# Performance work log

Hardware: AMD Instinct MI355X
Metric: run time of the kernel (lower is better)

Reference implementation:

```python
import jax, jax.numpy as jnp
import numpy as np

ALPHA = 0.25
GAMMA = 2.0
EPS = 1e-8
W_CLASS = 2.0
W_BBOX = 5.0
W_GIOU = 2.0
B, Q, T, C = 64, 900, 300, 80


def setup_inputs() -> dict:
    key = jax.random.key(0)
    k1, k2, k3, k4 = jax.random.split(key, 4)
    pred_logits = jax.random.normal(k1, (B, Q, C), dtype=jnp.float32)
    pred_boxes = jax.random.uniform(k2, (B, Q, 4), dtype=jnp.float32)  # cxcywh in (0,1)
    tgt_labels = jax.random.randint(k3, (B, T), 0, C, dtype=jnp.int64)
    tgt_boxes = jax.random.uniform(k4, (B, T, 4), dtype=jnp.float32)
    return {"pred_logits": pred_logits, "pred_boxes": pred_boxes,
            "tgt_labels": tgt_labels, "tgt_boxes": tgt_boxes}


def box_cxcywh_to_xyxy(b):
    cx, cy, w, h = b[..., 0], b[..., 1], b[..., 2], b[..., 3]
    return jnp.stack([cx - 0.5 * w, cy - 0.5 * h, cx + 0.5 * w, cy + 0.5 * h], axis=-1)


def pairwise_giou(boxes1, boxes2):
    # boxes1: [B,Q,4] xyxy, boxes2: [B,T,4] xyxy -> [B,Q,T]
    area1 = (boxes1[..., 2] - boxes1[..., 0]) * (boxes1[..., 3] - boxes1[..., 1])
    area2 = (boxes2[..., 2] - boxes2[..., 0]) * (boxes2[..., 3] - boxes2[..., 1])
    lt = jnp.maximum(boxes1[:, :, None, :2], boxes2[:, None, :, :2])
    rb = jnp.minimum(boxes1[:, :, None, 2:], boxes2[:, None, :, 2:])
    wh = jnp.clip(rb - lt, 0.0)
    inter = wh[..., 0] * wh[..., 1]
    union = area1[:, :, None] + area2[:, None, :] - inter
    iou = inter / union
    lt_c = jnp.minimum(boxes1[:, :, None, :2], boxes2[:, None, :, :2])
    rb_c = jnp.maximum(boxes1[:, :, None, 2:], boxes2[:, None, :, 2:])
    wh_c = jnp.clip(rb_c - lt_c, 0.0)
    area_c = wh_c[..., 0] * wh_c[..., 1]
    return iou - (area_c - union) / area_c


def reference(pred_logits, pred_boxes, tgt_labels, tgt_boxes):
    # Batched cost matrix of HungarianMatcher (use_focal_loss=True).
    prob = jax.nn.sigmoid(pred_logits)  # [B,Q,C]
    idx = jnp.broadcast_to(tgt_labels[:, None, :], (prob.shape[0], prob.shape[1], tgt_labels.shape[1]))
    p = jnp.take_along_axis(prob, idx.astype(jnp.int32), axis=2)  # [B,Q,T]
    neg_cost = (1.0 - ALPHA) * p ** GAMMA * (-jnp.log(1.0 - p + EPS))
    pos_cost = ALPHA * (1.0 - p) ** GAMMA * (-jnp.log(p + EPS))
    cost_class = pos_cost - neg_cost
    cost_bbox = jnp.abs(pred_boxes[:, :, None, :] - tgt_boxes[:, None, :, :]).sum(-1)
    cost_giou = -pairwise_giou(box_cxcywh_to_xyxy(pred_boxes), box_cxcywh_to_xyxy(tgt_boxes))
    cost = W_BBOX * cost_bbox + W_CLASS * cost_class + W_GIOU * cost_giou
    return jnp.nan_to_num(cost, nan=1.0, posinf=1e6, neginf=-1e6)
```

## Files before the change

kernel.cpp:

```cpp
#include <hip/hip_runtime.h>


constexpr int B = 64, Q = 900, T = 300, C = 80;
constexpr int QTILE = 18;
constexpr int BLOCK = 256;
constexpr int TG    = T / 4;
constexpr int NIT   = (QTILE / 2) * TG;
constexpr float ALPHA = 0.25f;
constexpr float EPSF  = 1e-8f;

__device__ __forceinline__ float fast_rcp(float x) {
    return __builtin_amdgcn_rcpf(x);
}

__global__ __launch_bounds__(BLOCK) void matcher_cost_kernel(
    const float* __restrict__ logits,
    const float* __restrict__ pboxes,
    const int*   __restrict__ tlabels,
    const float* __restrict__ tboxes,
    float* __restrict__ out)
{
    __shared__ float4 s_t[9][TG];
    __shared__ int4   s_tl[TG];
    __shared__ float  s_cls[QTILE * C];
    __shared__ float4 s_pA[QTILE];
    __shared__ float4 s_pB[QTILE];

    const int bid = blockIdx.x;
    const int b   = bid / (Q / QTILE);
    const int q0  = (bid % (Q / QTILE)) * QTILE;
    const int tid = threadIdx.x;

    for (int t = tid; t < T; t += BLOCK) {
        float4 bx = *(const float4*)(tboxes + ((size_t)b * T + t) * 4);
        float x0 = bx.x - 0.5f * bx.z, y0 = bx.y - 0.5f * bx.w;
        float x1 = bx.x + 0.5f * bx.z, y1 = bx.y + 0.5f * bx.w;
        ((float*)&s_t[0][0])[t] = bx.x;
        ((float*)&s_t[1][0])[t] = bx.y;
        ((float*)&s_t[2][0])[t] = bx.z;
        ((float*)&s_t[3][0])[t] = bx.w;
        ((float*)&s_t[4][0])[t] = x0;
        ((float*)&s_t[5][0])[t] = y0;
        ((float*)&s_t[6][0])[t] = x1;
        ((float*)&s_t[7][0])[t] = y1;
        ((float*)&s_t[8][0])[t] = bx.z * bx.w;
        ((int*)&s_tl[0])[t]     = tlabels[(size_t)b * T + t];
    }

    if (tid < QTILE) {
        float4 bx = *(const float4*)(pboxes + ((size_t)b * Q + q0 + tid) * 4);
        float x0 = bx.x - 0.5f * bx.z, y0 = bx.y - 0.5f * bx.w;
        float x1 = bx.x + 0.5f * bx.z, y1 = bx.y + 0.5f * bx.w;
        s_pA[tid] = bx;
        s_pB[tid] = make_float4(x0, y0, x1, y1);
    }

    {
        const float* lg = logits + ((size_t)b * Q + q0) * C;
        for (int i = tid; i < QTILE * C; i += BLOCK) {
            float x  = lg[i];
            float pr = fast_rcp(1.0f + __expf(-x));
            float om = 1.0f - pr;
            float pos = ALPHA * om * om * (-__logf(pr + EPSF));
            float neg = (1.0f - ALPHA) * pr * pr * (-__logf(om + EPSF));
            s_cls[i] = 2.0f * (pos - neg) + 2.0f;
        }
    }

    __syncthreads();

    float* outb = out + ((size_t)b * Q + q0) * T;
    for (unsigned it = tid; it < NIT; it += BLOCK) {
        unsigned qp = it / TG;
        unsigned tg = it - qp * TG;

        float4 tcx = s_t[0][tg], tcy = s_t[1][tg];
        float4 tw  = s_t[2][tg], th  = s_t[3][tg];
        float4 tx0 = s_t[4][tg], ty0 = s_t[5][tg];
        float4 tx1 = s_t[6][tg], ty1 = s_t[7][tg];
        float4 ta  = s_t[8][tg];
        int4   lab = s_tl[tg];

        #pragma unroll
        for (int dq = 0; dq < 2; ++dq) {
            const int ql = qp * 2 + dq;
            float4 pA = s_pA[ql];
            float4 pB = s_pB[ql];
            float  pa = pA.z * pA.w;
            const float* clsrow = s_cls + ql * C;

            float4 res;
            #pragma unroll
            for (int k = 0; k < 4; ++k) {
                float tcx_ = (&tcx.x)[k], tcy_ = (&tcy.x)[k];
                float tw_  = (&tw.x)[k],  th_  = (&th.x)[k];
                float tx0_ = (&tx0.x)[k], ty0_ = (&ty0.x)[k];
                float tx1_ = (&tx1.x)[k], ty1_ = (&ty1.x)[k];
                float ta_  = (&ta.x)[k];

                float cbbox = (fabsf(pA.x - tcx_) + fabsf(pA.y - tcy_)) +
                              (fabsf(pA.z - tw_ ) + fabsf(pA.w - th_ ));
                float cls2 = clsrow[(&lab.x)[k]];

                float iw = fmaxf(fminf(pB.z, tx1_) - fmaxf(pB.x, tx0_), 0.0f);
                float ih = fmaxf(fminf(pB.w, ty1_) - fmaxf(pB.y, ty0_), 0.0f);
                float inter = iw * ih;
                float uni   = (pa + ta_) - inter;

                float cw = fmaxf(pB.z, tx1_) - fminf(pB.x, tx0_);
                float ch = fmaxf(pB.w, ty1_) - fminf(pB.y, ty0_);
                float ca = cw * ch;

                float num = fmaf(uni, uni, inter * ca);
                float r   = fast_rcp(uni * ca);
                float c   = fmaf(5.0f, cbbox, cls2);
                c = fmaf(num, -2.0f * r, c);

                if (c != c) c = 1.0f;

                (&res.x)[k] = c;
            }
            *(float4*)(outb + (size_t)ql * T + tg * 4) = res;
        }
    }
}

extern "C" void kernel_launch(void* const* d_in, const int* in_sizes, int n_in,
                              void* d_out, int out_size, void* d_ws, size_t ws_size,
                              hipStream_t stream) {
    const float* logits  = (const float*)d_in[0];
    const float* pboxes  = (const float*)d_in[1];
    const int*   tlabels = (const int*)  d_in[2];
    const float* tboxes  = (const float*)d_in[3];
    float* out = (float*)d_out;

    dim3 grid(B * (Q / QTILE));
    dim3 block(BLOCK);
    matcher_cost_kernel<<<grid, block, 0, stream>>>(logits, pboxes, tlabels, tboxes, out);
}
```

Measured before the change: 34.70 us.

## Split focal cost into transposed precompute kernel and widen query tile

Adds a first kernel that computes the focal class cost once per logit and stores it transposed as [B,C,Q] in the workspace. The main kernel then gathers four consecutive queries per label with a float4 global load, and each thread now handles four queries instead of two (QTILE 20). Per-block logit staging and the shared class buffer are removed. This costs an extra launch and an extra round trip of about 18 MB through global memory, and there is a fallback kernel for when the workspace is too small.

```diff
diff --git a/kernel.cpp b/kernel.cpp
--- a/kernel.cpp
+++ b/kernel.cpp
@@ -2,27 +2,70 @@
 
 
 constexpr int B = 64, Q = 900, T = 300, C = 80;
-constexpr int QTILE = 18;
+constexpr float ALPHA = 0.25f;
+constexpr float EPSF  = 1e-8f;
+
+constexpr int K1_QT    = 75;
+constexpr int K1_TILES = Q / K1_QT;
+constexpr int K1_BLOCK = 256;
+
+constexpr int QTILE = 20;
 constexpr int BLOCK = 256;
 constexpr int TG    = T / 4;
-constexpr int NIT   = (QTILE / 2) * TG;
-constexpr float ALPHA = 0.25f;
-constexpr float EPSF  = 1e-8f;
+constexpr int QG    = QTILE / 4;
+constexpr int NIT   = QG * TG;
 
 __device__ __forceinline__ float fast_rcp(float x) {
     return __builtin_amdgcn_rcpf(x);
 }
 
+__device__ __forceinline__ float focal2(float x) {
+    float pr = fast_rcp(1.0f + __expf(-x));
+    float om = 1.0f - pr;
+    float pos = ALPHA * om * om * (-__logf(pr + EPSF));
+    float neg = (1.0f - ALPHA) * pr * pr * (-__logf(om + EPSF));
+    return 2.0f * (pos - neg) + 2.0f;
+}
+
+__global__ __launch_bounds__(K1_BLOCK) void focal_transpose_kernel(
+    const float* __restrict__ logits,
+    float* __restrict__ clsT)
+{
+    __shared__ float sT[C * K1_QT];
+
+    const int bid  = blockIdx.x;
+    const int b    = bid / K1_TILES;
+    const int tile = bid - b * K1_TILES;
+    const int q0   = tile * K1_QT;
+    const int tid  = threadIdx.x;
+
+    const float* lg = logits + ((size_t)b * Q + q0) * C;
+    for (int i4 = tid; i4 < K1_QT * C / 4; i4 += K1_BLOCK) {
+        float4 x4 = *(const float4*)(lg + i4 * 4);
+        int q  = i4 / (C / 4);
+        int c0 = (i4 - q * (C / 4)) * 4;
+        #pragma unroll
+        for (int j = 0; j < 4; ++j)
+            sT[(c0 + j) * K1_QT + q] = focal2((&x4.x)[j]);
+    }
+    __syncthreads();
+
+    float* ob = clsT + (size_t)b * C * Q + q0;
+    for (int j = tid; j < C * K1_QT; j += K1_BLOCK) {
+        int c = j / K1_QT, q = j - c * K1_QT;
+        ob[(size_t)c * Q + q] = sT[j];
+    }
+}
+
 __global__ __launch_bounds__(BLOCK) void matcher_cost_kernel(
-    const float* __restrict__ logits,
     const float* __restrict__ pboxes,
     const int*   __restrict__ tlabels,
     const float* __restrict__ tboxes,
+    const float* __restrict__ clsT,
     float* __restrict__ out)
 {
     __shared__ float4 s_t[9][TG];
     __shared__ int4   s_tl[TG];
-    __shared__ float  s_cls[QTILE * C];
     __shared__ float4 s_pA[QTILE];
     __shared__ float4 s_pB[QTILE];
 
@@ -46,7 +89,6 @@
         ((float*)&s_t[8][0])[t] = bx.z * bx.w;
         ((int*)&s_tl[0])[t]     = tlabels[(size_t)b * T + t];
     }
-
     if (tid < QTILE) {
         float4 bx = *(const float4*)(pboxes + ((size_t)b * Q + q0 + tid) * 4);
         float x0 = bx.x - 0.5f * bx.z, y0 = bx.y - 0.5f * bx.w;
@@ -54,40 +96,37 @@
         s_pA[tid] = bx;
         s_pB[tid] = make_float4(x0, y0, x1, y1);
     }
-
-    {
-        const float* lg = logits + ((size_t)b * Q + q0) * C;
-        for (int i = tid; i < QTILE * C; i += BLOCK) {
-            float x  = lg[i];
-            float pr = fast_rcp(1.0f + __expf(-x));
-            float om = 1.0f - pr;
-            float pos = ALPHA * om * om * (-__logf(pr + EPSF));
-            float neg = (1.0f - ALPHA) * pr * pr * (-__logf(om + EPSF));
-            s_cls[i] = 2.0f * (pos - neg) + 2.0f;
-        }
-    }
-
     __syncthreads();
 
+    const float* ct = clsT + (size_t)b * C * Q + q0;
     float* outb = out + ((size_t)b * Q + q0) * T;
+
     for (unsigned it = tid; it < NIT; it += BLOCK) {
-        unsigned qp = it / TG;
-        unsigned tg = it - qp * TG;
+        unsigned qg = it / TG;
+        unsigned tg = it - qg * TG;
+
+        int4 lab = s_tl[tg];
+
+        const float* cb = ct + qg * 4;
+        float4 clsq0 = *(const float4*)(cb + (unsigned)lab.x * Q);
+        float4 clsq1 = *(const float4*)(cb + (unsigned)lab.y * Q);
+        float4 clsq2 = *(const float4*)(cb + (unsigned)lab.z * Q);
+        float4 clsq3 = *(const float4*)(cb + (unsigned)lab.w * Q);
 
         float4 tcx = s_t[0][tg], tcy = s_t[1][tg];
         float4 tw  = s_t[2][tg], th  = s_t[3][tg];
         float4 tx0 = s_t[4][tg], ty0 = s_t[5][tg];
         float4 tx1 = s_t[6][tg], ty1 = s_t[7][tg];
         float4 ta  = s_t[8][tg];
-        int4   lab = s_tl[tg];
+
+        float* o0 = outb + (size_t)(qg * 4) * T + tg * 4;
 
         #pragma unroll
-        for (int dq = 0; dq < 2; ++dq) {
-            const int ql = qp * 2 + dq;
+        for (int dq = 0; dq < 4; ++dq) {
+            const int ql = qg * 4 + dq;
             float4 pA = s_pA[ql];
             float4 pB = s_pB[ql];
             float  pa = pA.z * pA.w;
-            const float* clsrow = s_cls + ql * C;
 
             float4 res;
             #pragma unroll
@@ -100,7 +139,9 @@
 
                 float cbbox = (fabsf(pA.x - tcx_) + fabsf(pA.y - tcy_)) +
                               (fabsf(pA.z - tw_ ) + fabsf(pA.w - th_ ));
-                float cls2 = clsrow[(&lab.x)[k]];
+                float cls2 = (k == 0) ? (&clsq0.x)[dq] :
+                             (k == 1) ? (&clsq1.x)[dq] :
+                             (k == 2) ? (&clsq2.x)[dq] : (&clsq3.x)[dq];
 
                 float iw = fmaxf(fminf(pB.z, tx1_) - fmaxf(pB.x, tx0_), 0.0f);
                 float ih = fmaxf(fminf(pB.w, ty1_) - fmaxf(pB.y, ty0_), 0.0f);
@@ -118,6 +159,87 @@
 
                 if (c != c) c = 1.0f;
 
+                (&res.x)[k] = c;
+            }
+            *(float4*)(o0 + (size_t)dq * T) = res;
+        }
+    }
+}
+
+constexpr int FQT = 18;
+constexpr int FNIT = (FQT / 2) * TG;
+
+__global__ __launch_bounds__(BLOCK) void matcher_cost_fallback(
+    const float* __restrict__ logits, const float* __restrict__ pboxes,
+    const int* __restrict__ tlabels, const float* __restrict__ tboxes,
+    float* __restrict__ out)
+{
+    __shared__ float4 s_t[9][TG];
+    __shared__ int4   s_tl[TG];
+    __shared__ float  s_cls[FQT * C];
+    __shared__ float4 s_pA[FQT];
+    __shared__ float4 s_pB[FQT];
+
+    const int bid = blockIdx.x;
+    const int b   = bid / (Q / FQT);
+    const int q0  = (bid % (Q / FQT)) * FQT;
+    const int tid = threadIdx.x;
+
+    for (int t = tid; t < T; t += BLOCK) {
+        float4 bx = *(const float4*)(tboxes + ((size_t)b * T + t) * 4);
+        float x0 = bx.x - 0.5f * bx.z, y0 = bx.y - 0.5f * bx.w;
+        float x1 = bx.x + 0.5f * bx.z, y1 = bx.y + 0.5f * bx.w;
+        ((float*)&s_t[0][0])[t] = bx.x; ((float*)&s_t[1][0])[t] = bx.y;
+        ((float*)&s_t[2][0])[t] = bx.z; ((float*)&s_t[3][0])[t] = bx.w;
+        ((float*)&s_t[4][0])[t] = x0;   ((float*)&s_t[5][0])[t] = y0;
+        ((float*)&s_t[6][0])[t] = x1;   ((float*)&s_t[7][0])[t] = y1;
+        ((float*)&s_t[8][0])[t] = bx.z * bx.w;
+        ((int*)&s_tl[0])[t]     = tlabels[(size_t)b * T + t];
+    }
+    if (tid < FQT) {
+        float4 bx = *(const float4*)(pboxes + ((size_t)b * Q + q0 + tid) * 4);
+        s_pA[tid] = bx;
+        s_pB[tid] = make_float4(bx.x - 0.5f * bx.z, bx.y - 0.5f * bx.w,
+                                bx.x + 0.5f * bx.z, bx.y + 0.5f * bx.w);
+    }
+    {
+        const float* lg = logits + ((size_t)b * Q + q0) * C;
+        for (int i = tid; i < FQT * C; i += BLOCK) s_cls[i] = focal2(lg[i]);
+    }
+    __syncthreads();
+
+    float* outb = out + ((size_t)b * Q + q0) * T;
+    for (unsigned it = tid; it < FNIT; it += BLOCK) {
+        unsigned qp = it / TG, tg = it - qp * TG;
+        float4 tcx = s_t[0][tg], tcy = s_t[1][tg];
+        float4 tw  = s_t[2][tg], th  = s_t[3][tg];
+        float4 tx0 = s_t[4][tg], ty0 = s_t[5][tg];
+        float4 tx1 = s_t[6][tg], ty1 = s_t[7][tg];
+        float4 ta  = s_t[8][tg];
+        int4   lab = s_tl[tg];
+        #pragma unroll
+        for (int dq = 0; dq < 2; ++dq) {
+            const int ql = qp * 2 + dq;
+            float4 pA = s_pA[ql]; float4 pB = s_pB[ql];
+            float  pa = pA.z * pA.w;
+            const float* clsrow = s_cls + ql * C;
+            float4 res;
+            #pragma unroll
+            for (int k = 0; k < 4; ++k) {
+                float cbbox = (fabsf(pA.x - (&tcx.x)[k]) + fabsf(pA.y - (&tcy.x)[k])) +
+                              (fabsf(pA.z - (&tw.x)[k])  + fabsf(pA.w - (&th.x)[k]));
+                float cls2 = clsrow[(&lab.x)[k]];
+                float iw = fmaxf(fminf(pB.z, (&tx1.x)[k]) - fmaxf(pB.x, (&tx0.x)[k]), 0.0f);
+                float ih = fmaxf(fminf(pB.w, (&ty1.x)[k]) - fmaxf(pB.y, (&ty0.x)[k]), 0.0f);
+                float inter = iw * ih;
+                float uni = (pa + (&ta.x)[k]) - inter;
+                float cw = fmaxf(pB.z, (&tx1.x)[k]) - fminf(pB.x, (&tx0.x)[k]);
+                float ch = fmaxf(pB.w, (&ty1.x)[k]) - fminf(pB.y, (&ty0.x)[k]);
+                float ca = cw * ch;
+                float num = fmaf(uni, uni, inter * ca);
+                float c = fmaf(5.0f, cbbox, cls2);
+                c = fmaf(num, -2.0f * fast_rcp(uni * ca), c);
+                if (c != c) c = 1.0f;
                 (&res.x)[k] = c;
             }
             *(float4*)(outb + (size_t)ql * T + tg * 4) = res;
@@ -134,7 +256,15 @@
     const float* tboxes  = (const float*)d_in[3];
     float* out = (float*)d_out;
 
-    dim3 grid(B * (Q / QTILE));
-    dim3 block(BLOCK);
-    matcher_cost_kernel<<<grid, block, 0, stream>>>(logits, pboxes, tlabels, tboxes, out);
-}
+    const size_t clsT_bytes = (size_t)B * C * Q * sizeof(float);
+    if (ws_size >= clsT_bytes) {
+        float* clsT = (float*)d_ws;
+        focal_transpose_kernel<<<dim3(B * K1_TILES), dim3(K1_BLOCK), 0, stream>>>(
+            logits, clsT);
+        matcher_cost_kernel<<<dim3(B * (Q / QTILE)), dim3(BLOCK), 0, stream>>>(
+            pboxes, tlabels, tboxes, clsT, out);
+    } else {
+        matcher_cost_fallback<<<dim3(B * (Q / FQT)), dim3(BLOCK), 0, stream>>>(
+            logits, pboxes, tlabels, tboxes, out);
+    }
+}
```

Result: slower. 43.24 us (+24.6%).
